# Performance work log

Hardware: AMD Instinct MI355X
Metric: run time of the kernel (lower is better)

## Reference

```python
import jax, jax.numpy as jnp
import numpy as np

N = 50000
IN_C = 128
OUT_C = 64


def gcn_conv(x, edge_index, W, b):
    # PyG GCNConv: h = X W; add self-loops; symmetric norm D^-1/2 (A+I) D^-1/2; aggregate; + bias
    n = x.shape[0]
    h = x @ W  # [N, out]
    loop = jnp.arange(n, dtype=edge_index.dtype)
    row = jnp.concatenate([edge_index[0], loop])  # source
    col = jnp.concatenate([edge_index[1], loop])  # target
    deg = jax.ops.segment_sum(jnp.ones_like(col, dtype=h.dtype), col, num_segments=n)
    dinv = jnp.where(deg > 0, jax.lax.rsqrt(deg), 0.0)
    norm = dinv[row] * dinv[col]  # [E+N]
    msg = norm[:, None] * h[row]  # gather source features
    out = jax.ops.segment_sum(msg, col, num_segments=n)  # scatter to targets
    return out + b


def layer_norm(x, w, b, eps=1e-5):
    mu = jnp.mean(x, axis=-1, keepdims=True)
    var = jnp.mean((x - mu) ** 2, axis=-1, keepdims=True)
    return (x - mu) * jax.lax.rsqrt(var + eps) * w + b


def setup_inputs() -> dict:
    key = jax.random.key(0)
    ks = jax.random.split(key, 10)
    x = jax.random.normal(ks[0], (N, IN_C), dtype=jnp.float32)
    edge_index = jax.random.randint(ks[1], (2, 800000), 0, N, dtype=jnp.int64)
    s1 = 1.0 / np.sqrt(IN_C)
    s2 = 1.0 / np.sqrt(OUT_C)
    W1 = jax.random.uniform(ks[2], (IN_C, OUT_C), jnp.float32, -s1, s1)
    b1 = jnp.zeros((OUT_C,), jnp.float32)
    ln_w = jnp.ones((OUT_C,), jnp.float32)
    ln_b = jnp.zeros((OUT_C,), jnp.float32)
    W2 = jax.random.uniform(ks[3], (OUT_C, OUT_C), jnp.float32, -s2, s2)
    b2 = jnp.zeros((OUT_C,), jnp.float32)
    W3 = jax.random.uniform(ks[4], (OUT_C, 6), jnp.float32, -s2, s2)
    b3 = jax.random.uniform(ks[5], (6,), jnp.float32, -s2, s2)
    return {"x": x, "edge_index": edge_index, "W1": W1, "b1": b1,
            "ln_w": ln_w, "ln_b": ln_b, "W2": W2, "b2": b2, "W3": W3, "b3": b3}


def reference(x, edge_index, W1, b1, ln_w, ln_b, W2, b2, W3, b3):
    h = gcn_conv(x, edge_index, W1, b1)           # [N, 64]
    h = jax.nn.relu(layer_norm(h, ln_w, ln_b))    # [N, 64]
    out1 = gcn_conv(h, edge_index, W2, b2)        # [N, 64]
    out2 = jax.nn.sigmoid(h @ W3 + b3)            # [N, 6]
    return (out1, out2)
```

## Files before the change

### kernel.cpp

```cpp
#include <hip/hip_runtime.h>
#include <hip/hip_fp16.h>
#include <math.h>


#define ELLW 48

typedef _Float16 half8 __attribute__((ext_vector_type(8)));
typedef float f32x4 __attribute__((ext_vector_type(4)));

__global__ void k_init(int* __restrict__ cnt, int n) {
    int i = blockIdx.x * blockDim.x + threadIdx.x;
    if (i < n) cnt[i] = 0;
}

__global__ void k_scatter(const int* __restrict__ row, const int* __restrict__ col,
                          int* __restrict__ cnt, int* __restrict__ ell, int E) {
    int e = blockIdx.x * blockDim.x + threadIdx.x;
    if (e < E) {
        int c = col[e];
        int r = atomicAdd(&cnt[c], 1);
        if (r < ELLW) ell[c * ELLW + r] = row[e] << 7;
    }
}

__global__ void k_dinv(const int* __restrict__ cnt, float* __restrict__ dinv, int n) {
    int i = blockIdx.x * blockDim.x + threadIdx.x;
    if (i < n) dinv[i] = rsqrtf((float)(cnt[i] + 1));
}

__global__ void k_pack(const float* __restrict__ W1, const float* __restrict__ W2,
                       const float* __restrict__ W3, _Float16* __restrict__ W1g,
                       _Float16* __restrict__ Bg) {
    int idx = blockIdx.x * 256 + threadIdx.x;
    if (idx < 8192) {
        int j = idx & 7, L = (idx >> 3) & 63, s = (idx >> 9) & 3, t = idx >> 11;
        int k = s * 32 + (L >> 4) * 8 + j;
        int c = t * 16 + (L & 15);
        W1g[idx] = (_Float16)W1[k * 64 + c];
    } else if (idx < 8192 + 5120) {
        int i2 = idx - 8192;
        int j = i2 & 7, L = (i2 >> 3) & 63, s = (i2 >> 9) & 1, u = i2 >> 10;
        int k = s * 32 + (L >> 4) * 8 + j;
        int c = (L & 15);
        float v;
        if (u < 4) v = W2[k * 64 + u * 16 + c];
        else v = (c < 6) ? W3[k * 6 + c] : 0.f;
        Bg[i2] = (_Float16)v;
    }
}

__global__ __launch_bounds__(256, 4) void k_gemm1(
    const float* __restrict__ x, const _Float16* __restrict__ W1g,
    const float* __restrict__ dinv, uint* __restrict__ hs,
    uint* __restrict__ h2s, int n) {
    int tid = threadIdx.x;
    if (blockIdx.x == 0) {
        if (tid < 32) hs[(size_t)n * 32 + tid] = 0u;
        else if (tid < 64) h2s[(size_t)n * 32 + (tid - 32)] = 0u;
    }
    int lane = tid & 63, wid = tid >> 6;
    int m16 = lane & 15, quad = lane >> 4;
    int node0 = blockIdx.x * 64 + wid * 16;
    int arow = node0 + m16;
    if (arow >= n) arow = n - 1;
    const float* xr = x + (size_t)arow * 128;
    half8 A[4];
#pragma unroll
    for (int s = 0; s < 4; s++) {
        const float4* p = (const float4*)(xr + s * 32 + quad * 8);
        float4 f0 = p[0], f1 = p[1];
        half8 a;
        a[0] = (_Float16)f0.x; a[1] = (_Float16)f0.y;
        a[2] = (_Float16)f0.z; a[3] = (_Float16)f0.w;
        a[4] = (_Float16)f1.x; a[5] = (_Float16)f1.y;
        a[6] = (_Float16)f1.z; a[7] = (_Float16)f1.w;
        A[s] = a;
    }
    float dsc[4];
#pragma unroll
    for (int r = 0; r < 4; r++) {
        int nd = node0 + quad * 4 + r;
        dsc[r] = dinv[nd < n ? nd : n - 1];
    }
    const half8* Wv = (const half8*)W1g;
#pragma unroll
    for (int t = 0; t < 4; t++) {
        f32x4 acc = {0.f, 0.f, 0.f, 0.f};
#pragma unroll
        for (int s = 0; s < 4; s++)
            acc = __builtin_amdgcn_mfma_f32_16x16x32_f16(A[s], Wv[(t * 4 + s) * 64 + lane], acc, 0, 0, 0);
#pragma unroll
        for (int r = 0; r < 4; r++) {
            int nd = node0 + quad * 4 + r;
            float v = acc[r] * dsc[r];
            float vo = __shfl_xor(v, 1, 64);
            if (!(m16 & 1) && nd < n) {
                __half2 pk = __floats2half2_rn(v, vo);
                hs[(size_t)nd * 32 + t * 8 + (m16 >> 1)] = *(uint*)&pk;
            }
        }
    }
}

#define GATHER_BODY(SRC)                                                      \
    int4 o1[4], o2[4];                                                        \
    uint4 u0[4], u1[4];                                                       \
    {                                                                         \
        int4 o0[4];                                                           \
        _Pragma("unroll") for (int p = 0; p < 4; p++) o0[p] = ldidx(p, 0);    \
        _Pragma("unroll") for (int p = 0; p < 4; p++) o1[p] = ldidx(p, 8);    \
        _Pragma("unroll") for (int p = 0; p < 4; p++) {                       \
            u0[p].x = *(const uint*)(SRC + o0[p].x + m4);                     \
            u0[p].y = *(const uint*)(SRC + o0[p].y + m4);                     \
            u0[p].z = *(const uint*)(SRC + o0[p].z + m4);                     \
            u0[p].w = *(const uint*)(SRC + o0[p].w + m4);                     \
        }                                                                     \
    }                                                                         \
    for (int jb = 0; jb < Pmax; jb += 8) {                                    \
        _Pragma("unroll") for (int p = 0; p < 4; p++) o2[p] = ldidx(p, jb + 16); \
        _Pragma("unroll") for (int p = 0; p < 4; p++) {                       \
            u1[p].x = *(const uint*)(SRC + o1[p].x + m4);                     \
            u1[p].y = *(const uint*)(SRC + o1[p].y + m4);                     \
            u1[p].z = *(const uint*)(SRC + o1[p].z + m4);                     \
            u1[p].w = *(const uint*)(SRC + o1[p].w + m4);                     \
        }                                                                     \
        _Pragma("unroll") for (int p = 0; p < 4; p++) {                       \
            float2 f;                                                         \
            f = __half22float2(*(__half2*)&u0[p].x); ax[p] += f.x; ay[p] += f.y; \
            f = __half22float2(*(__half2*)&u0[p].y); ax[p] += f.x; ay[p] += f.y; \
            f = __half22float2(*(__half2*)&u0[p].z); ax[p] += f.x; ay[p] += f.y; \
            f = __half22float2(*(__half2*)&u0[p].w); ax[p] += f.x; ay[p] += f.y; \
        }                                                                     \
        _Pragma("unroll") for (int p = 0; p < 4; p++) { o1[p] = o2[p]; u0[p] = u1[p]; } \
    }

__global__ __launch_bounds__(256, 4) void k_conv1_fused(
    const uint* __restrict__ hs, const int* __restrict__ ell,
    const int* __restrict__ cnt, const float* __restrict__ dinv,
    const float* __restrict__ b1, const float* __restrict__ lnw_g,
    const float* __restrict__ lnb_g, const _Float16* __restrict__ Bg,
    const float* __restrict__ b3, uint* __restrict__ h2s,
    float* __restrict__ out2, int zoff, int n) {
    __shared__ _Float16 Y[4][16 * 72];
    int tid = threadIdx.x;
    int lane = tid & 63, wid = tid >> 6;
    int m = lane & 31, g = lane >> 5;
    int m4 = m * 4;
    {
        float4 z = {0.f, 0.f, 0.f, 0.f};
        float4* yb = (float4*)Y[wid];
        for (int i = lane; i < 144; i += 64) yb[i] = z;
    }
    int base = blockIdx.x * 16;
    int nid[4], st[4], P[4];
    int Pmax = 0;
#pragma unroll
    for (int p = 0; p < 4; p++) {
        int node = base + wid * 4 + p;
        if (node >= n) node = n - 1;
        nid[p] = node;
        st[p] = node * ELLW;
        P[p] = cnt[node];
        Pmax = Pmax > P[p] ? Pmax : P[p];
    }
    Pmax = (Pmax + 7) & ~7;
    auto ldidx = [&](int p, int jb) -> int4 {
        int4 o = *(const int4*)(ell + st[p] + jb + 4 * g);
        int b = jb + 4 * g;
        o.x = (b + 0 < P[p]) ? o.x : zoff;
        o.y = (b + 1 < P[p]) ? o.y : zoff;
        o.z = (b + 2 < P[p]) ? o.z : zoff;
        o.w = (b + 3 < P[p]) ? o.w : zoff;
        return o;
    };
    const char* hsb = (const char*)hs;
    float ax[4], ay[4];
#pragma unroll
    for (int p = 0; p < 4; p++) {
        int sa = (g == 0) ? (nid[p] << 7) : zoff;
        uint us = *(const uint*)(hsb + sa + m4);
        float2 f = __half22float2(*(__half2*)&us);
        ax[p] = f.x; ay[p] = f.y;
    }
    GATHER_BODY(hsb)

    float2 b1v = ((const float2*)b1)[m];
    float2 lw = ((const float2*)lnw_g)[m];
    float2 lb = ((const float2*)lnb_g)[m];
    float dcs[4];
#pragma unroll
    for (int p = 0; p < 4; p++) {
        float axp = ax[p] + __shfl_xor(ax[p], 32, 64);
        float ayp = ay[p] + __shfl_xor(ay[p], 32, 64);
        float dc = dinv[nid[p]];
        dcs[p] = dc;
        float va = fmaf(dc, axp, b1v.x);
        float vb = fmaf(dc, ayp, b1v.y);
        float s = va + vb;
#pragma unroll
        for (int off = 16; off > 0; off >>= 1) s += __shfl_xor(s, off, 64);
        float mu = s * (1.f / 64.f);
        float da = va - mu, db = vb - mu;
        float q = da * da + db * db;
#pragma unroll
        for (int off = 16; off > 0; off >>= 1) q += __shfl_xor(q, off, 64);
        float rstd = rsqrtf(q * (1.f / 64.f) + 1e-5f);
        float yA = fmaxf(fmaf(da * rstd, lw.x, lb.x), 0.f);
        float yB = fmaxf(fmaf(db * rstd, lw.y, lb.y), 0.f);
        if (g == 0) {
            __half2 pk = __floats2half2_rn(yA, yB);
            *(__half2*)&Y[wid][p * 72 + 2 * m] = pk;
        }
    }
    int m16 = lane & 15, quad = lane >> 4;
    half8 a0 = *(const half8*)&Y[wid][m16 * 72 + quad * 8];
    half8 a1 = *(const half8*)&Y[wid][m16 * 72 + 32 + quad * 8];
    const half8* Bv = (const half8*)Bg;
    _Float16* h2h = (_Float16*)h2s;
#pragma unroll
    for (int t = 0; t < 4; t++) {
        f32x4 acc = {0.f, 0.f, 0.f, 0.f};
        acc = __builtin_amdgcn_mfma_f32_16x16x32_f16(a0, Bv[(t * 2 + 0) * 64 + lane], acc, 0, 0, 0);
        acc = __builtin_amdgcn_mfma_f32_16x16x32_f16(a1, Bv[(t * 2 + 1) * 64 + lane], acc, 0, 0, 0);
#pragma unroll
        for (int r = 0; r < 4; r++) {
            int nodep = base + wid * 4 + r;
            if (quad == 0 && nodep < n)
                h2h[(size_t)nodep * 64 + t * 16 + m16] = (_Float16)(acc[r] * dcs[r]);
        }
    }
    {
        f32x4 acc = {0.f, 0.f, 0.f, 0.f};
        acc = __builtin_amdgcn_mfma_f32_16x16x32_f16(a0, Bv[8 * 64 + lane], acc, 0, 0, 0);
        acc = __builtin_amdgcn_mfma_f32_16x16x32_f16(a1, Bv[9 * 64 + lane], acc, 0, 0, 0);
        float bb = b3[m16 < 6 ? m16 : 0];
#pragma unroll
        for (int r = 0; r < 4; r++) {
            int nodep = base + wid * 4 + r;
            if (quad == 0 && m16 < 6 && nodep < n)
                out2[(size_t)nodep * 6 + m16] = 1.f / (1.f + __expf(-(acc[r] + bb)));
        }
    }
}

__global__ __launch_bounds__(256, 4) void k_conv2(
    const uint* __restrict__ h2s, const int* __restrict__ ell,
    const int* __restrict__ cnt, const float* __restrict__ dinv,
    const float* __restrict__ b2, float* __restrict__ out1, int zoff, int n) {
    int tid = threadIdx.x;
    int lane = tid & 63, wid = tid >> 6;
    int m = lane & 31, g = lane >> 5;
    int m4 = m * 4;
    int base = blockIdx.x * 16;
    int nid[4], st[4], P[4];
    int Pmax = 0;
#pragma unroll
    for (int p = 0; p < 4; p++) {
        int node = base + wid * 4 + p;
        if (node >= n) node = n - 1;
        nid[p] = node;
        st[p] = node * ELLW;
        P[p] = cnt[node];
        Pmax = Pmax > P[p] ? Pmax : P[p];
    }
    Pmax = (Pmax + 7) & ~7;
    auto ldidx = [&](int p, int jb) -> int4 {
        int4 o = *(const int4*)(ell + st[p] + jb + 4 * g);
        int b = jb + 4 * g;
        o.x = (b + 0 < P[p]) ? o.x : zoff;
        o.y = (b + 1 < P[p]) ? o.y : zoff;
        o.z = (b + 2 < P[p]) ? o.z : zoff;
        o.w = (b + 3 < P[p]) ? o.w : zoff;
        return o;
    };
    const char* hsb = (const char*)h2s;
    float ax[4], ay[4];
#pragma unroll
    for (int p = 0; p < 4; p++) {
        int sa = (g == 0) ? (nid[p] << 7) : zoff;
        uint us = *(const uint*)(hsb + sa + m4);
        float2 f = __half22float2(*(__half2*)&us);
        ax[p] = f.x; ay[p] = f.y;
    }
    GATHER_BODY(hsb)

    float2 b2v = ((const float2*)b2)[m];
#pragma unroll
    for (int p = 0; p < 4; p++) {
        float axp = ax[p] + __shfl_xor(ax[p], 32, 64);
        float ayp = ay[p] + __shfl_xor(ay[p], 32, 64);
        int node = base + wid * 4 + p;
        if (g == 0 && node < n) {
            float dc = dinv[nid[p]];
            float2 r;
            r.x = fmaf(dc, axp, b2v.x);
            r.y = fmaf(dc, ayp, b2v.y);
            ((float2*)out1)[(size_t)node * 32 + m] = r;
        }
    }
}

extern "C" void kernel_launch(void* const* d_in, const int* in_sizes, int n_in,
                              void* d_out, int out_size, void* d_ws, size_t ws_size,
                              hipStream_t stream) {
    const float* x   = (const float*)d_in[0];
    const int*   ei  = (const int*)d_in[1];
    const float* W1  = (const float*)d_in[2];
    const float* b1  = (const float*)d_in[3];
    const float* lnw = (const float*)d_in[4];
    const float* lnb = (const float*)d_in[5];
    const float* W2  = (const float*)d_in[6];
    const float* b2  = (const float*)d_in[7];
    const float* W3  = (const float*)d_in[8];
    const float* b3  = (const float*)d_in[9];

    int n = in_sizes[0] / 128;
    int E = in_sizes[1] / 2;
    const int* row = ei;
    const int* col = ei + E;

    char* ws = (char*)d_ws;
    size_t off = 0;
    auto carve = [&](size_t bytes) -> char* {
        char* p = ws + off;
        off = (off + bytes + 255) & ~(size_t)255;
        return p;
    };
    int*   cnt  = (int*)carve(4 * (size_t)n);
    float* dinv = (float*)carve(4 * (size_t)n);
    int*   ell  = (int*)carve(4 * ((size_t)n * ELLW + 256));
    uint*  hs   = (uint*)carve(128 * ((size_t)n + 1));
    uint*  h2s  = (uint*)carve(128 * ((size_t)n + 1));
    _Float16* W1g = (_Float16*)carve(2 * 8192);
    _Float16* Bg  = (_Float16*)carve(2 * 5120);

    float* out1 = (float*)d_out;
    float* out2 = out1 + (size_t)n * 64;
    int zero_off = n << 7;

    k_pack<<<52, 256, 0, stream>>>(W1, W2, W3, W1g, Bg);
    k_init<<<(n + 255) / 256, 256, 0, stream>>>(cnt, n);
    k_scatter<<<(E + 255) / 256, 256, 0, stream>>>(row, col, cnt, ell, E);
    k_dinv<<<(n + 255) / 256, 256, 0, stream>>>(cnt, dinv, n);
    k_gemm1<<<(n + 63) / 64, 256, 0, stream>>>(x, W1g, dinv, hs, h2s, n);
    k_conv1_fused<<<(n + 15) / 16, 256, 0, stream>>>(hs, ell, cnt, dinv,
                                                     b1, lnw, lnb, Bg, b3,
                                                     h2s, out2, zero_off, n);
    k_conv2<<<(n + 15) / 16, 256, 0, stream>>>(h2s, ell, cnt, dinv, b2,
                                               out1, zero_off, n);
}
```

Before: 204.7 us.

## Overlap edge scatter with first GEMM and apply degree scaling afterward

Merges the ELL scatter and the first feature GEMM into one launch. The first 512 blocks build the ELL lists, each block reading a slice of edges and keeping only targets in one of eight node partitions, which is meant to localise the atomics. The remaining blocks compute X·W1 without the degree scale. A new pass then computes dinv, rescales the stored fp16 features in place and zeroes the padding rows. This removes the dependency of the GEMM on the scatter so the two can run concurrently, but each edge is now read eight times and the features take an extra read/write pass plus an extra fp16 rounding.

Measured after the change: 208.7 us. Within noise of the previous version (+2.0%).

```diff
diff --git a/kernel.cpp b/kernel.cpp
--- a/kernel.cpp
+++ b/kernel.cpp
@@ -4,6 +4,7 @@
 
 
 #define ELLW 48
+#define NSCAT 512
 
 typedef _Float16 half8 __attribute__((ext_vector_type(8)));
 typedef float f32x4 __attribute__((ext_vector_type(4)));
@@ -11,21 +12,6 @@
 __global__ void k_init(int* __restrict__ cnt, int n) {
     int i = blockIdx.x * blockDim.x + threadIdx.x;
     if (i < n) cnt[i] = 0;
-}
-
-__global__ void k_scatter(const int* __restrict__ row, const int* __restrict__ col,
-                          int* __restrict__ cnt, int* __restrict__ ell, int E) {
-    int e = blockIdx.x * blockDim.x + threadIdx.x;
-    if (e < E) {
-        int c = col[e];
-        int r = atomicAdd(&cnt[c], 1);
-        if (r < ELLW) ell[c * ELLW + r] = row[e] << 7;
-    }
-}
-
-__global__ void k_dinv(const int* __restrict__ cnt, float* __restrict__ dinv, int n) {
-    int i = blockIdx.x * blockDim.x + threadIdx.x;
-    if (i < n) dinv[i] = rsqrtf((float)(cnt[i] + 1));
 }
 
 __global__ void k_pack(const float* __restrict__ W1, const float* __restrict__ W2,
@@ -49,18 +35,33 @@
     }
 }
 
-__global__ __launch_bounds__(256, 4) void k_gemm1(
+__global__ __launch_bounds__(256) void k_scatter_gemm(
+    const int* __restrict__ row, const int* __restrict__ col,
+    int* __restrict__ cnt, int* __restrict__ ell,
     const float* __restrict__ x, const _Float16* __restrict__ W1g,
-    const float* __restrict__ dinv, uint* __restrict__ hs,
-    uint* __restrict__ h2s, int n) {
+    uint* __restrict__ hs, int E, int n, int psize) {
+    if (blockIdx.x < NSCAT) {
+        int part = blockIdx.x & 7;
+        int slice = blockIdx.x >> 3;
+        const int nslice = NSCAT / 8;
+        int per = (E + nslice - 1) / nslice;
+        int e0 = slice * per;
+        int e1 = e0 + per; if (e1 > E) e1 = E;
+        int pl = part * psize;
+        int ph = pl + psize; if (ph > n) ph = n;
+        for (int e = e0 + (int)threadIdx.x; e < e1; e += 256) {
+            int c = col[e];
+            if (c >= pl && c < ph) {
+                int r = atomicAdd(&cnt[c], 1);
+                if (r < ELLW) ell[c * ELLW + r] = row[e] << 7;
+            }
+        }
+        return;
+    }
     int tid = threadIdx.x;
-    if (blockIdx.x == 0) {
-        if (tid < 32) hs[(size_t)n * 32 + tid] = 0u;
-        else if (tid < 64) h2s[(size_t)n * 32 + (tid - 32)] = 0u;
-    }
     int lane = tid & 63, wid = tid >> 6;
     int m16 = lane & 15, quad = lane >> 4;
-    int node0 = blockIdx.x * 64 + wid * 16;
+    int node0 = (blockIdx.x - NSCAT) * 64 + wid * 16;
     int arow = node0 + m16;
     if (arow >= n) arow = n - 1;
     const float* xr = x + (size_t)arow * 128;
@@ -76,12 +77,6 @@
         a[6] = (_Float16)f1.z; a[7] = (_Float16)f1.w;
         A[s] = a;
     }
-    float dsc[4];
-#pragma unroll
-    for (int r = 0; r < 4; r++) {
-        int nd = node0 + quad * 4 + r;
-        dsc[r] = dinv[nd < n ? nd : n - 1];
-    }
     const half8* Wv = (const half8*)W1g;
 #pragma unroll
     for (int t = 0; t < 4; t++) {
@@ -92,7 +87,7 @@
 #pragma unroll
         for (int r = 0; r < 4; r++) {
             int nd = node0 + quad * 4 + r;
-            float v = acc[r] * dsc[r];
+            float v = acc[r];
             float vo = __shfl_xor(v, 1, 64);
             if (!(m16 & 1) && nd < n) {
                 __half2 pk = __floats2half2_rn(v, vo);
@@ -100,6 +95,20 @@
             }
         }
     }
+}
+
+__global__ void k_dinv_scale(const int* __restrict__ cnt, float* __restrict__ dinv,
+                             uint* __restrict__ hs, uint* __restrict__ h2s, int n) {
+    int idx = blockIdx.x * 256 + threadIdx.x;
+    if (idx >= (n + 1) * 32) return;
+    int node = idx >> 5;
+    if (node >= n) { hs[idx] = 0u; h2s[idx] = 0u; return; }
+    float s = rsqrtf((float)(cnt[node] + 1));
+    if ((idx & 31) == 0) dinv[node] = s;
+    uint u = hs[idx];
+    float2 f = __half22float2(*(__half2*)&u);
+    __half2 pk = __floats2half2_rn(s * f.x, s * f.y);
+    hs[idx] = *(uint*)&pk;
 }
 
 #define GATHER_BODY(SRC)                                                      \
@@ -337,12 +346,13 @@
     float* out1 = (float*)d_out;
     float* out2 = out1 + (size_t)n * 64;
     int zero_off = n << 7;
+    int psize = (n + 7) / 8;
 
     k_pack<<<52, 256, 0, stream>>>(W1, W2, W3, W1g, Bg);
     k_init<<<(n + 255) / 256, 256, 0, stream>>>(cnt, n);
-    k_scatter<<<(E + 255) / 256, 256, 0, stream>>>(row, col, cnt, ell, E);
-    k_dinv<<<(n + 255) / 256, 256, 0, stream>>>(cnt, dinv, n);
-    k_gemm1<<<(n + 63) / 64, 256, 0, stream>>>(x, W1g, dinv, hs, h2s, n);
+    k_scatter_gemm<<<NSCAT + (n + 63) / 64, 256, 0, stream>>>(
+        row, col, cnt, ell, x, W1g, hs, E, n, psize);
+    k_dinv_scale<<<((n + 1) * 32 + 255) / 256, 256, 0, stream>>>(cnt, dinv, hs, h2s, n);
     k_conv1_fused<<<(n + 15) / 16, 256, 0, stream>>>(hs, ell, cnt, dinv,
                                                      b1, lnw, lnb, Bg, b3,
                                                      h2s, out2, zero_off, n);
```

## Split feature tables into half-width planes and aggregate in two passes

Applied to the files above, without the earlier changes.

Stores the fp16 hidden features as two 32-channel planes (64 bytes per node), so each gather pass touches a smaller table that fits the cache better. Each aggregation is run twice, once per plane, with 16 lanes per row and 16 neighbors per iteration. The first conv is split into an aggregation kernel that writes fp32 results to a workspace, then a separate finish kernel for layernorm and the GEMMs. The cost is extra launches, an fp32 intermediate round trip through memory, and reading the neighbor index lists twice.

Measured after the change: 235.7 us. +15.1%, slower.

```diff
diff --git a/kernel.cpp b/kernel.cpp
--- a/kernel.cpp
+++ b/kernel.cpp
@@ -19,7 +19,7 @@
     if (e < E) {
         int c = col[e];
         int r = atomicAdd(&cnt[c], 1);
-        if (r < ELLW) ell[c * ELLW + r] = row[e] << 7;
+        if (r < ELLW) ell[c * ELLW + r] = row[e] << 6;
     }
 }
 
@@ -52,11 +52,12 @@
 __global__ __launch_bounds__(256, 4) void k_gemm1(
     const float* __restrict__ x, const _Float16* __restrict__ W1g,
     const float* __restrict__ dinv, uint* __restrict__ hs,
-    uint* __restrict__ h2s, int n) {
+    uint* __restrict__ h2s, int n, int pstride ) {
     int tid = threadIdx.x;
-    if (blockIdx.x == 0) {
-        if (tid < 32) hs[(size_t)n * 32 + tid] = 0u;
-        else if (tid < 64) h2s[(size_t)n * 32 + (tid - 32)] = 0u;
+    if (blockIdx.x == 0 && tid < 64) {
+        int q = tid >> 4, w = tid & 15;
+        uint* dst = (q < 2) ? hs : h2s;
+        dst[(size_t)(q & 1) * pstride + (size_t)n * 16 + w] = 0u;
     }
     int lane = tid & 63, wid = tid >> 6;
     int m16 = lane & 15, quad = lane >> 4;
@@ -89,6 +90,7 @@
 #pragma unroll
         for (int s = 0; s < 4; s++)
             acc = __builtin_amdgcn_mfma_f32_16x16x32_f16(A[s], Wv[(t * 4 + s) * 64 + lane], acc, 0, 0, 0);
+        uint* hp = hs + (size_t)(t >> 1) * pstride;
 #pragma unroll
         for (int r = 0; r < 4; r++) {
             int nd = node0 + quad * 4 + r;
@@ -96,19 +98,19 @@
             float vo = __shfl_xor(v, 1, 64);
             if (!(m16 & 1) && nd < n) {
                 __half2 pk = __floats2half2_rn(v, vo);
-                hs[(size_t)nd * 32 + t * 8 + (m16 >> 1)] = *(uint*)&pk;
+                hp[(size_t)nd * 16 + (t & 1) * 8 + (m16 >> 1)] = *(uint*)&pk;
             }
         }
     }
 }
 
-#define GATHER_BODY(SRC)                                                      \
+#define GATHER16(SRC)                                                         \
     int4 o1[4], o2[4];                                                        \
     uint4 u0[4], u1[4];                                                       \
     {                                                                         \
         int4 o0[4];                                                           \
         _Pragma("unroll") for (int p = 0; p < 4; p++) o0[p] = ldidx(p, 0);    \
-        _Pragma("unroll") for (int p = 0; p < 4; p++) o1[p] = ldidx(p, 8);    \
+        _Pragma("unroll") for (int p = 0; p < 4; p++) o1[p] = ldidx(p, 16);   \
         _Pragma("unroll") for (int p = 0; p < 4; p++) {                       \
             u0[p].x = *(const uint*)(SRC + o0[p].x + m4);                     \
             u0[p].y = *(const uint*)(SRC + o0[p].y + m4);                     \
@@ -116,7 +118,7 @@
             u0[p].w = *(const uint*)(SRC + o0[p].w + m4);                     \
         }                                                                     \
     }                                                                         \
-    for (int jb = 0; jb < Pmax; jb += 8) {                                    \
+    for (int jb = 16; jb < Pmax; jb += 16) {                                  \
         _Pragma("unroll") for (int p = 0; p < 4; p++) o2[p] = ldidx(p, jb + 16); \
         _Pragma("unroll") for (int p = 0; p < 4; p++) {                       \
             u1[p].x = *(const uint*)(SRC + o1[p].x + m4);                     \
@@ -132,70 +134,100 @@
             f = __half22float2(*(__half2*)&u0[p].w); ax[p] += f.x; ay[p] += f.y; \
         }                                                                     \
         _Pragma("unroll") for (int p = 0; p < 4; p++) { o1[p] = o2[p]; u0[p] = u1[p]; } \
-    }
-
-__global__ __launch_bounds__(256, 4) void k_conv1_fused(
-    const uint* __restrict__ hs, const int* __restrict__ ell,
+    }                                                                         \
+    _Pragma("unroll") for (int p = 0; p < 4; p++) {                           \
+        float2 f;                                                             \
+        f = __half22float2(*(__half2*)&u0[p].x); ax[p] += f.x; ay[p] += f.y;  \
+        f = __half22float2(*(__half2*)&u0[p].y); ax[p] += f.x; ay[p] += f.y;  \
+        f = __half22float2(*(__half2*)&u0[p].z); ax[p] += f.x; ay[p] += f.y;  \
+        f = __half22float2(*(__half2*)&u0[p].w); ax[p] += f.x; ay[p] += f.y;  \
+    }                                                                         \
+    _Pragma("unroll") for (int p = 0; p < 4; p++) {                           \
+        ax[p] += __shfl_xor(ax[p], 16, 64); ay[p] += __shfl_xor(ay[p], 16, 64); \
+        ax[p] += __shfl_xor(ax[p], 32, 64); ay[p] += __shfl_xor(ay[p], 32, 64); \
+    }
+
+#define GATHER_PRE(SEEDSRC)                                                   \
+    int base = blockIdx.x * 16;                                               \
+    int nid[4], st[4], P[4];                                                  \
+    int Pmax = 0;                                                             \
+    _Pragma("unroll") for (int p = 0; p < 4; p++) {                           \
+        int node = base + wid * 4 + p;                                        \
+        if (node >= n) node = n - 1;                                          \
+        nid[p] = node;                                                        \
+        st[p] = node * ELLW;                                                  \
+        int c = cnt[node]; P[p] = c < ELLW ? c : ELLW;                        \
+        Pmax = Pmax > P[p] ? Pmax : P[p];                                     \
+    }                                                                         \
+    Pmax = (Pmax + 15) & ~15;                                                 \
+    auto ldidx = [&](int p, int jb) -> int4 {                                 \
+        int4 o = *(const int4*)(ell + st[p] + jb + 4 * g4);                   \
+        int b = jb + 4 * g4;                                                  \
+        o.x = (b + 0 < P[p]) ? o.x : zoff;                                    \
+        o.y = (b + 1 < P[p]) ? o.y : zoff;                                    \
+        o.z = (b + 2 < P[p]) ? o.z : zoff;                                    \
+        o.w = (b + 3 < P[p]) ? o.w : zoff;                                    \
+        return o;                                                             \
+    };                                                                        \
+    float ax[4], ay[4];                                                       \
+    _Pragma("unroll") for (int p = 0; p < 4; p++) {                           \
+        int sa = (g4 == 0) ? (nid[p] << 6) : zoff;                            \
+        uint us = *(const uint*)((SEEDSRC) + sa + m4);                        \
+        float2 f = __half22float2(*(__half2*)&us);                            \
+        ax[p] = f.x; ay[p] = f.y;                                             \
+    }
+
+__global__ __launch_bounds__(256, 4) void k_agg(
+    const uint* __restrict__ hsq, const int* __restrict__ ell,
     const int* __restrict__ cnt, const float* __restrict__ dinv,
-    const float* __restrict__ b1, const float* __restrict__ lnw_g,
-    const float* __restrict__ lnb_g, const _Float16* __restrict__ Bg,
-    const float* __restrict__ b3, uint* __restrict__ h2s,
-    float* __restrict__ out2, int zoff, int n) {
+    const float* __restrict__ bq, float* __restrict__ aggq,
+    int zoff, int n) {
+    int tid = threadIdx.x;
+    int lane = tid & 63, wid = tid >> 6;
+    int m16 = lane & 15, g4 = (lane >> 4) & 3;
+    int m4 = m16 * 4;
+    const char* hsb = (const char*)hsq;
+    GATHER_PRE(hsb)
+    GATHER16(hsb)
+    float2 bb = ((const float2*)bq)[m16];
+#pragma unroll
+    for (int p = 0; p < 4; p++) {
+        int node = base + wid * 4 + p;
+        if (lane < 16 && node < n) {
+            float dc = dinv[nid[p]];
+            float2 r;
+            r.x = fmaf(dc, ax[p], bb.x);
+            r.y = fmaf(dc, ay[p], bb.y);
+            ((float2*)(aggq + (size_t)node * 64))[m16] = r;
+        }
+    }
+}
+
+__global__ __launch_bounds__(256, 4) void k_finish(
+    const float* __restrict__ agg, const float* __restrict__ dinv,
+    const float* __restrict__ lnw_g, const float* __restrict__ lnb_g,
+    const _Float16* __restrict__ Bg, const float* __restrict__ b3,
+    uint* __restrict__ h2s, float* __restrict__ out2, int n, int pstride) {
     __shared__ _Float16 Y[4][16 * 72];
     int tid = threadIdx.x;
     int lane = tid & 63, wid = tid >> 6;
     int m = lane & 31, g = lane >> 5;
-    int m4 = m * 4;
     {
         float4 z = {0.f, 0.f, 0.f, 0.f};
         float4* yb = (float4*)Y[wid];
         for (int i = lane; i < 144; i += 64) yb[i] = z;
     }
     int base = blockIdx.x * 16;
-    int nid[4], st[4], P[4];
-    int Pmax = 0;
+    float2 lw = ((const float2*)lnw_g)[m];
+    float2 lb = ((const float2*)lnb_g)[m];
+    float dcs[4];
 #pragma unroll
     for (int p = 0; p < 4; p++) {
         int node = base + wid * 4 + p;
         if (node >= n) node = n - 1;
-        nid[p] = node;
-        st[p] = node * ELLW;
-        P[p] = cnt[node];
-        Pmax = Pmax > P[p] ? Pmax : P[p];
-    }
-    Pmax = (Pmax + 7) & ~7;
-    auto ldidx = [&](int p, int jb) -> int4 {
-        int4 o = *(const int4*)(ell + st[p] + jb + 4 * g);
-        int b = jb + 4 * g;
-        o.x = (b + 0 < P[p]) ? o.x : zoff;
-        o.y = (b + 1 < P[p]) ? o.y : zoff;
-        o.z = (b + 2 < P[p]) ? o.z : zoff;
-        o.w = (b + 3 < P[p]) ? o.w : zoff;
-        return o;
-    };
-    const char* hsb = (const char*)hs;
-    float ax[4], ay[4];
-#pragma unroll
-    for (int p = 0; p < 4; p++) {
-        int sa = (g == 0) ? (nid[p] << 7) : zoff;
-        uint us = *(const uint*)(hsb + sa + m4);
-        float2 f = __half22float2(*(__half2*)&us);
-        ax[p] = f.x; ay[p] = f.y;
-    }
-    GATHER_BODY(hsb)
-
-    float2 b1v = ((const float2*)b1)[m];
-    float2 lw = ((const float2*)lnw_g)[m];
-    float2 lb = ((const float2*)lnb_g)[m];
-    float dcs[4];
-#pragma unroll
-    for (int p = 0; p < 4; p++) {
-        float axp = ax[p] + __shfl_xor(ax[p], 32, 64);
-        float ayp = ay[p] + __shfl_xor(ay[p], 32, 64);
-        float dc = dinv[nid[p]];
-        dcs[p] = dc;
-        float va = fmaf(dc, axp, b1v.x);
-        float vb = fmaf(dc, ayp, b1v.y);
+        dcs[p] = dinv[node];
+        float2 v = ((const float2*)(agg + (size_t)node * 64))[m];
+        float va = v.x, vb = v.y;
         float s = va + vb;
 #pragma unroll
         for (int off = 16; off > 0; off >>= 1) s += __shfl_xor(s, off, 64);
@@ -222,11 +254,12 @@
         f32x4 acc = {0.f, 0.f, 0.f, 0.f};
         acc = __builtin_amdgcn_mfma_f32_16x16x32_f16(a0, Bv[(t * 2 + 0) * 64 + lane], acc, 0, 0, 0);
         acc = __builtin_amdgcn_mfma_f32_16x16x32_f16(a1, Bv[(t * 2 + 1) * 64 + lane], acc, 0, 0, 0);
+        _Float16* hp = h2h + (size_t)(t >> 1) * 2 * pstride;
 #pragma unroll
         for (int r = 0; r < 4; r++) {
             int nodep = base + wid * 4 + r;
             if (quad == 0 && nodep < n)
-                h2h[(size_t)nodep * 64 + t * 16 + m16] = (_Float16)(acc[r] * dcs[r]);
+                hp[(size_t)nodep * 32 + (t & 1) * 16 + m16] = (_Float16)(acc[r] * dcs[r]);
         }
     }
     {
@@ -244,58 +277,27 @@
 }
 
 __global__ __launch_bounds__(256, 4) void k_conv2(
-    const uint* __restrict__ h2s, const int* __restrict__ ell,
+    const uint* __restrict__ h2q, const int* __restrict__ ell,
     const int* __restrict__ cnt, const float* __restrict__ dinv,
-    const float* __restrict__ b2, float* __restrict__ out1, int zoff, int n) {
+    const float* __restrict__ bq, float* __restrict__ out1q,
+    int zoff, int n) {
     int tid = threadIdx.x;
     int lane = tid & 63, wid = tid >> 6;
-    int m = lane & 31, g = lane >> 5;
-    int m4 = m * 4;
-    int base = blockIdx.x * 16;
-    int nid[4], st[4], P[4];
-    int Pmax = 0;
+    int m16 = lane & 15, g4 = (lane >> 4) & 3;
+    int m4 = m16 * 4;
+    const char* hsb = (const char*)h2q;
+    GATHER_PRE(hsb)
+    GATHER16(hsb)
+    float2 bb = ((const float2*)bq)[m16];
 #pragma unroll
     for (int p = 0; p < 4; p++) {
         int node = base + wid * 4 + p;
-        if (node >= n) node = n - 1;
-        nid[p] = node;
-        st[p] = node * ELLW;
-        P[p] = cnt[node];
-        Pmax = Pmax > P[p] ? Pmax : P[p];
-    }
-    Pmax = (Pmax + 7) & ~7;
-    auto ldidx = [&](int p, int jb) -> int4 {
-        int4 o = *(const int4*)(ell + st[p] + jb + 4 * g);
-        int b = jb + 4 * g;
-        o.x = (b + 0 < P[p]) ? o.x : zoff;
-        o.y = (b + 1 < P[p]) ? o.y : zoff;
-        o.z = (b + 2 < P[p]) ? o.z : zoff;
-        o.w = (b + 3 < P[p]) ? o.w : zoff;
-        return o;
-    };
-    const char* hsb = (const char*)h2s;
-    float ax[4], ay[4];
-#pragma unroll
-    for (int p = 0; p < 4; p++) {
-        int sa = (g == 0) ? (nid[p] << 7) : zoff;
-        uint us = *(const uint*)(hsb + sa + m4);
-        float2 f = __half22float2(*(__half2*)&us);
-        ax[p] = f.x; ay[p] = f.y;
-    }
-    GATHER_BODY(hsb)
-
-    float2 b2v = ((const float2*)b2)[m];
-#pragma unroll
-    for (int p = 0; p < 4; p++) {
-        float axp = ax[p] + __shfl_xor(ax[p], 32, 64);
-        float ayp = ay[p] + __shfl_xor(ay[p], 32, 64);
-        int node = base + wid * 4 + p;
-        if (g == 0 && node < n) {
+        if (lane < 16 && node < n) {
             float dc = dinv[nid[p]];
             float2 r;
-            r.x = fmaf(dc, axp, b2v.x);
-            r.y = fmaf(dc, ayp, b2v.y);
-            ((float2*)out1)[(size_t)node * 32 + m] = r;
+            r.x = fmaf(dc, ax[p], bb.x);
+            r.y = fmaf(dc, ay[p], bb.y);
+            ((float2*)(out1q + (size_t)node * 64))[m16] = r;
         }
     }
 }
@@ -326,26 +328,29 @@
         off = (off + bytes + 255) & ~(size_t)255;
         return p;
     };
+    int pstride = (n + 1) * 16;
     int*   cnt  = (int*)carve(4 * (size_t)n);
     float* dinv = (float*)carve(4 * (size_t)n);
     int*   ell  = (int*)carve(4 * ((size_t)n * ELLW + 256));
-    uint*  hs   = (uint*)carve(128 * ((size_t)n + 1));
-    uint*  h2s  = (uint*)carve(128 * ((size_t)n + 1));
+    uint*  hs   = (uint*)carve(4 * 2 * (size_t)pstride);
+    uint*  h2s  = (uint*)carve(4 * 2 * (size_t)pstride);
+    float* agg  = (float*)carve(4 * 64 * (size_t)n);
     _Float16* W1g = (_Float16*)carve(2 * 8192);
     _Float16* Bg  = (_Float16*)carve(2 * 5120);
 
     float* out1 = (float*)d_out;
     float* out2 = out1 + (size_t)n * 64;
-    int zero_off = n << 7;
+    int zoff = n << 6;
+    int nb16 = (n + 15) / 16;
 
     k_pack<<<52, 256, 0, stream>>>(W1, W2, W3, W1g, Bg);
     k_init<<<(n + 255) / 256, 256, 0, stream>>>(cnt, n);
     k_scatter<<<(E + 255) / 256, 256, 0, stream>>>(row, col, cnt, ell, E);
     k_dinv<<<(n + 255) / 256, 256, 0, stream>>>(cnt, dinv, n);
-    k_gemm1<<<(n + 63) / 64, 256, 0, stream>>>(x, W1g, dinv, hs, h2s, n);
-    k_conv1_fused<<<(n + 15) / 16, 256, 0, stream>>>(hs, ell, cnt, dinv,
-                                                     b1, lnw, lnb, Bg, b3,
-                                                     h2s, out2, zero_off, n);
-    k_conv2<<<(n + 15) / 16, 256, 0, stream>>>(h2s, ell, cnt, dinv, b2,
-                                               out1, zero_off, n);
-}
+    k_gemm1<<<(n + 63) / 64, 256, 0, stream>>>(x, W1g, dinv, hs, h2s, n, pstride);
+    k_agg<<<nb16, 256, 0, stream>>>(hs,            ell, cnt, dinv, b1,      agg,      zoff, n);
+    k_agg<<<nb16, 256, 0, stream>>>(hs + pstride,  ell, cnt, dinv, b1 + 32, agg + 32, zoff, n);
+    k_finish<<<nb16, 256, 0, stream>>>(agg, dinv, lnw, lnb, Bg, b3, h2s, out2, n, pstride);
+    k_conv2<<<nb16, 256, 0, stream>>>(h2s,           ell, cnt, dinv, b2,      out1,      zoff, n);
+    k_conv2<<<nb16, 256, 0, stream>>>(h2s + pstride, ell, cnt, dinv, b2 + 32, out1 + 32, zoff, n);
+}
```
